# Kernel tuning notes

Measured on AMD Instinct MI355X. Metric: run time of the kernel, lower is better.

Reference implementation:

```python
import jax, jax.numpy as jnp
import numpy as np

D_MODEL, H, KV, HD = 2048, 32, 8, 64  # head_dim = 64, RoPE half-dim = 32
B, L = 2, 2048
EPS = 1e-06


def apply_rope(t, cos, sin):
    # t: [b,l,h,hd]; cos/sin: [1,l,1,hd//2] (broadcast over batch and heads)
    dim = t.shape[-1] // 2
    cos = cos[..., :dim]
    sin = sin[..., :dim]
    x1, x2 = t[..., :dim], t[..., dim:]
    return jnp.concatenate([x1 * cos - x2 * sin, x2 * cos + x1 * sin], axis=-1)


def setup_inputs() -> dict:
    key = jax.random.key(0)
    ks = jax.random.split(key, 5)
    x = jax.random.normal(ks[0], (B, L, D_MODEL), dtype=jnp.float32)
    # true rotary tables, theta=10000
    half = HD // 2
    inv_freq = 1.0 / (10000.0 ** (jnp.arange(half, dtype=jnp.float32) / half))
    ang = jnp.arange(L, dtype=jnp.float32)[:, None] * inv_freq[None, :]  # [L, half]
    cos = jnp.cos(ang)[None, :, None, :]  # [1,L,1,half]
    sin = jnp.sin(ang)[None, :, None, :]
    s = 0.02
    Wq = jax.random.normal(ks[1], (D_MODEL, D_MODEL), dtype=jnp.float32) * s
    Wk = jax.random.normal(ks[2], (D_MODEL, KV * HD), dtype=jnp.float32) * s
    Wv = jax.random.normal(ks[3], (D_MODEL, KV * HD), dtype=jnp.float32) * s
    Wo = jax.random.normal(ks[4], (D_MODEL, D_MODEL), dtype=jnp.float32) * s
    return {"x": x, "cos": cos, "sin": sin, "Wq": Wq, "Wk": Wk, "Wv": Wv, "Wo": Wo}


def reference(x, cos, sin, Wq, Wk, Wv, Wo):
    b, l, _ = x.shape
    q = (x @ Wq).reshape(b, l, H, HD)
    k = (x @ Wk).reshape(b, l, KV, HD)
    v = (x @ Wv).reshape(b, l, KV, HD)
    q = apply_rope(q, cos, sin)
    k = apply_rope(k, cos[:, :, :KV, :], sin[:, :, :KV, :])
    # QK RMS-norm (qk_norm=True path), done in fp32
    q32 = q.astype(jnp.float32)
    k32 = k.astype(jnp.float32)
    q = (q32 * jax.lax.rsqrt(jnp.mean(jnp.square(q32), axis=-1, keepdims=True) + EPS)).astype(q.dtype)
    k = (k32 * jax.lax.rsqrt(jnp.mean(jnp.square(k32), axis=-1, keepdims=True) + EPS)).astype(k.dtype)
    # GQA: repeat KV heads to match Q heads
    g = H // KV
    k = jnp.repeat(k, g, axis=2)
    v = jnp.repeat(v, g, axis=2)
    scale = jax.lax.rsqrt(jnp.float32(HD))
    scores = jnp.einsum('blhd,bmhd->bhlm', q, k) * scale  # [b,H,L,L]
    causal = jnp.tril(jnp.ones((l, l), dtype=jnp.bool_))[None, None]
    scores = jnp.where(causal, scores, jnp.full_like(scores, -10000.0))
    attn = jax.nn.softmax(scores.astype(jnp.float32), axis=-1).astype(v.dtype)
    out = jnp.einsum('bhql,blhd->bqhd', attn, v).reshape(b, l, D_MODEL)
    return out @ Wo
```

## Files before the change

### kernel.cpp

```cpp
#include <hip/hip_runtime.h>
#include <hip/hip_bf16.h>
#include <cstdint>
#include <cstddef>

#define D_MODEL 2048
#define NH 32
#define NKV 8
#define HD 64
#define BB 2
#define LL 2048
#define EPS 1e-6f
#define MM (BB * LL)
#define QS 3072
#define KO 2048
#define VO 2560

typedef __hip_bfloat16 bf16;
typedef short bf16x8 __attribute__((ext_vector_type(8)));
typedef short s16x4 __attribute__((ext_vector_type(4)));
typedef float f32x4 __attribute__((ext_vector_type(4)));

__device__ inline float4 ld_bf4u(const unsigned short* p) {
  const ushort4 u = *(const ushort4*)p;
  float4 r;
  r.x = __uint_as_float(((unsigned)u.x) << 16);
  r.y = __uint_as_float(((unsigned)u.y) << 16);
  r.z = __uint_as_float(((unsigned)u.z) << 16);
  r.w = __uint_as_float(((unsigned)u.w) << 16);
  return r;
}
__device__ inline float4 ld4_rt(const void* p, size_t i, bool f32) {
  if (f32) return *(const float4*)((const float*)p + i);
  return ld_bf4u((const unsigned short*)p + i);
}
__device__ inline float ld1_rt(const void* p, size_t i, bool f32) {
  if (f32) return ((const float*)p)[i];
  unsigned short u = ((const unsigned short*)p)[i];
  return __uint_as_float(((unsigned)u) << 16);
}
__device__ inline unsigned short f2bf(float f) {
  bf16 h = __float2bfloat16(f);
  return *reinterpret_cast<unsigned short*>(&h);
}
__device__ inline float bfu2f(unsigned short u) {
  return __uint_as_float(((unsigned)u) << 16);
}
__device__ inline void store1(float* p, float v) { *p = v; }
__device__ inline void store1(unsigned short* p, float v) { *p = f2bf(v); }

__device__ inline void glds16(const unsigned short* g, unsigned short* l) {
  __builtin_amdgcn_global_load_lds(
      (const __attribute__((address_space(1))) unsigned int*)g,
      (__attribute__((address_space(3))) unsigned int*)l, 16, 0, 0);
}

__global__ __launch_bounds__(256) void detect_all(
    const unsigned short* p0, const unsigned short* p1, const unsigned short* p2,
    const unsigned short* p3, const unsigned short* p4, const unsigned short* p5,
    const unsigned short* p6, int* __restrict__ flags) {
  const unsigned short* ptrs[7] = {p0, p1, p2, p3, p4, p5, p6};
  const int b = blockIdx.x;
  const uint4* p = (const uint4*)ptrs[b];
  __shared__ int found;
  if (threadIdx.x == 0) found = 0;
  __syncthreads();
  int loc = 0;
#pragma unroll
  for (int it = 0; it < 16; ++it) {
    uint4 v = p[it * 256 + threadIdx.x];
    unsigned wds[4] = {v.x, v.y, v.z, v.w};
#pragma unroll
    for (int q = 0; q < 4; ++q) {
      unsigned lo = wds[q] & 0xFFFFu, hi = wds[q] >> 16;
      if (((lo >> 7) & 0xFFu) == 0xFFu || ((hi >> 7) & 0xFFu) == 0xFFu) loc = 1;
    }
  }
  if (loc) atomicOr(&found, 1);
  __syncthreads();
  if (threadIdx.x == 0) flags[b] = found;
}

__global__ __launch_bounds__(256) void cvt_bf16(const void* __restrict__ src,
                                                unsigned short* __restrict__ dst,
                                                int n4, const int* __restrict__ flags, int idx) {
  const bool f32 = flags[idx] != 0;
  int i = blockIdx.x * 256 + threadIdx.x;
  if (i < n4) {
    float4 v = ld4_rt(src, (size_t)i * 4, f32);
    ushort4 o;
    o.x = f2bf(v.x); o.y = f2bf(v.y); o.z = f2bf(v.z); o.w = f2bf(v.w);
    *(ushort4*)&dst[(size_t)i * 4] = o;
  }
}

__global__ __launch_bounds__(256) void transpose_any(const void* __restrict__ src,
                                                     unsigned short* __restrict__ dst,
                                                     int K, int N,
                                                     const int* __restrict__ flags, int idx) {
  const bool f32 = flags[idx] != 0;
  __shared__ unsigned short tile[64][65];
  const int t = threadIdx.x;
  const int n0 = blockIdx.x * 64, k0 = blockIdx.y * 64;
  const int cr = t >> 4, cc = (t & 15) * 4;
#pragma unroll
  for (int rr = 0; rr < 4; ++rr) {
    int row = rr * 16 + cr;
    float4 v = ld4_rt(src, (size_t)(k0 + row) * N + n0 + cc, f32);
    tile[row][cc + 0] = f2bf(v.x);
    tile[row][cc + 1] = f2bf(v.y);
    tile[row][cc + 2] = f2bf(v.z);
    tile[row][cc + 3] = f2bf(v.w);
  }
  __syncthreads();
#pragma unroll
  for (int rr = 0; rr < 4; ++rr) {
    int nrow = rr * 16 + cr;
    ushort4 o;
    o.x = tile[cc + 0][nrow];
    o.y = tile[cc + 1][nrow];
    o.z = tile[cc + 2][nrow];
    o.w = tile[cc + 3][nrow];
    *(ushort4*)&dst[(size_t)(n0 + nrow) * K + k0 + cc] = o;
  }
}

__global__ __launch_bounds__(256) void v_to_vt(const unsigned short* __restrict__ qkv,
                                               unsigned short* __restrict__ vt) {
  __shared__ unsigned short tile[64][72];
  const int t = threadIdx.x;
  const int l0 = blockIdx.x * 64;
  const int bk = blockIdx.y;
  const int r = t >> 2, c16 = (t & 3) * 16;
  const int b = bk >> 3, kvh = bk & 7;
  const unsigned short* src = &qkv[(size_t)(b * LL + l0 + r) * QS + VO + kvh * 64 + c16];
  *(uint4*)&tile[r][c16] = *(const uint4*)&src[0];
  *(uint4*)&tile[r][c16 + 8] = *(const uint4*)&src[8];
  __syncthreads();
  unsigned short u[16];
#pragma unroll
  for (int j = 0; j < 16; ++j) u[j] = tile[c16 + j][r];
  unsigned short* dst = &vt[((size_t)bk * 64 + r) * LL + l0 + c16];
  *(uint4*)&dst[0] = *(uint4*)&u[0];
  *(uint4*)&dst[8] = *(uint4*)&u[8];
}

template <typename CT, int FUSE>
__global__ __launch_bounds__(256) void gemm_mfma(const unsigned short* __restrict__ A,
                                                 const unsigned short* __restrict__ Bt,
                                                 CT* __restrict__ C,
                                                 int M, int N, int K, int lda,
                                                 const void* __restrict__ cosp,
                                                 const void* __restrict__ sinp,
                                                 const int* __restrict__ flags) {
  __shared__ __align__(16) unsigned short As[2][128 * 32];
  __shared__ __align__(16) unsigned short Bs[2][128 * 32];
  const int t = threadIdx.x;
  const int lane = t & 63, w = t >> 6;
  const int wm = (w >> 1) * 64, wn = (w & 1) * 64;
  const int g = lane >> 4, m16 = lane & 15;
  const int nwg = gridDim.x * gridDim.y;
  const int orig = blockIdx.y * gridDim.x + blockIdx.x;
  const int swz = (orig & 7) * (nwg >> 3) + (orig >> 3);
  const int m0 = (swz / gridDim.x) * 128, n0 = (swz % gridDim.x) * 128;
  const unsigned short* gA = &A[(size_t)(m0 + (t >> 2)) * lda + (t & 3) * 8];
  const unsigned short* gB = &Bt[(size_t)(n0 + (t >> 2)) * K + (t & 3) * 8];
  const int l8 = t * 8;
  f32x4 acc[4][4] = {};
  glds16(gA, &As[0][l8]);
  glds16(gA + (size_t)64 * lda, &As[0][l8 + 2048]);
  glds16(gB, &Bs[0][l8]);
  glds16(gB + (size_t)64 * K, &Bs[0][l8 + 2048]);
  __syncthreads();
  int cur = 0;
  for (int k0 = 0; k0 < K; k0 += 32) {
    if (k0 + 32 < K) {
      glds16(gA + k0 + 32, &As[cur ^ 1][l8]);
      glds16(gA + (size_t)64 * lda + k0 + 32, &As[cur ^ 1][l8 + 2048]);
      glds16(gB + k0 + 32, &Bs[cur ^ 1][l8]);
      glds16(gB + (size_t)64 * K + k0 + 32, &Bs[cur ^ 1][l8 + 2048]);
    }
    bf16x8 af[4], bfr[4];
#pragma unroll
    for (int i = 0; i < 4; ++i) af[i] = *(const bf16x8*)&As[cur][(wm + i * 16 + m16) * 32 + g * 8];
#pragma unroll
    for (int j = 0; j < 4; ++j) bfr[j] = *(const bf16x8*)&Bs[cur][(wn + j * 16 + m16) * 32 + g * 8];
#pragma unroll
    for (int i = 0; i < 4; ++i)
#pragma unroll
      for (int j = 0; j < 4; ++j)
        acc[i][j] = __builtin_amdgcn_mfma_f32_16x16x32_bf16(af[i], bfr[j], acc[i][j], 0, 0, 0);
    __syncthreads();
    cur ^= 1;
  }
  if constexpr (FUSE) {
    const int colbase = n0 + wn;
    if (colbase < VO) {
      const bool cf = flags[1] != 0, sf = flags[2] != 0;
#pragma unroll
      for (int i = 0; i < 4; ++i)
#pragma unroll
        for (int r = 0; r < 4; ++r) {
          const int row = m0 + wm + i * 16 + g * 4 + r;
          const int l = row & (LL - 1);
          const float c0 = ld1_rt(cosp, l * 32 + m16, cf);
          const float c1 = ld1_rt(cosp, l * 32 + 16 + m16, cf);
          const float s0 = ld1_rt(sinp, l * 32 + m16, sf);
          const float s1 = ld1_rt(sinp, l * 32 + 16 + m16, sf);
          const float x0 = acc[i][0][r], x1 = acc[i][1][r];
          const float x2 = acc[i][2][r], x3 = acc[i][3][r];
          const float r0 = x0 * c0 - x2 * s0;
          const float r1 = x1 * c1 - x3 * s1;
          const float r2 = x2 * c0 + x0 * s0;
          const float r3 = x3 * c1 + x1 * s1;
          float ss = r0 * r0 + r1 * r1 + r2 * r2 + r3 * r3;
#pragma unroll
          for (int off = 1; off < 16; off <<= 1) ss += __shfl_xor(ss, off);
          const float sc = rsqrtf(ss * (1.0f / HD) + EPS);
          CT* cr = &C[(size_t)row * N + colbase + m16];
          store1(cr + 0, r0 * sc);
          store1(cr + 16, r1 * sc);
          store1(cr + 32, r2 * sc);
          store1(cr + 48, r3 * sc);
        }
      return;
    }
  }
#pragma unroll
  for (int i = 0; i < 4; ++i)
#pragma unroll
    for (int j = 0; j < 4; ++j)
#pragma unroll
      for (int r = 0; r < 4; ++r) {
        int row = m0 + wm + i * 16 + g * 4 + r;
        int col = n0 + wn + j * 16 + m16;
        store1(&C[(size_t)row * N + col], acc[i][j][r]);
      }
}

__global__ __launch_bounds__(256) void attn_mfma(unsigned short* __restrict__ qkv,
                                                 const unsigned short* __restrict__ vt) {
  __shared__ __align__(16) unsigned short Ks[2][64 * 64];
  __shared__ __align__(16) unsigned short Vs[2][64 * 64];
  __shared__ __align__(16) unsigned short Pt[4][64 * 16];
  const int t = threadIdx.x, lane = t & 63, w = t >> 6;
  const int g = lane >> 4, m16 = lane & 15;
  const int h = blockIdx.x, b = blockIdx.y;
  const int qt = (LL / 64 - 1) - blockIdx.z;
  const int kvh = h >> 2;
  const int q0 = qt * 64, qr0 = q0 + w * 16;

  bf16x8 qf0, qf1;
  {
    const unsigned short* qrow = &qkv[(size_t)(b * LL + qr0 + m16) * QS + h * 64 + g * 8];
    qf0 = *(const bf16x8*)&qrow[0];
    qf1 = *(const bf16x8*)&qrow[32];
  }
  f32x4 Oacc[4] = {};
  float lrow[4] = {0.f, 0.f, 0.f, 0.f};

  const int lr = lane >> 3;
  const int lc = (lane & 7) ^ lr;
  const unsigned short* gK = &qkv[(size_t)(b * LL) * QS + KO + kvh * 64 + lc * 8];
  const unsigned short* gV = &vt[((size_t)(b * NKV + kvh) * 64 + w * 16 + lr) * LL + lc * 8];
  const int dbase = w * 1024 + lane * 8;
  const int nIter = q0 / 64 + 1;

#pragma unroll
  for (int c = 0; c < 2; ++c) {
    glds16(gK + (size_t)(w * 16 + c * 8 + lr) * QS, &Ks[0][dbase + c * 512]);
    glds16(gV + (size_t)c * 8 * LL, &Vs[0][dbase + c * 512]);
  }
  __syncthreads();

  const int sw8 = (m16 & 7) * 8;
  for (int it = 0; it < nIter; ++it) {
    const int j0 = it * 64;
    const int cur = it & 1;
    if (it + 1 < nIter) {
      const int nj = j0 + 64;
#pragma unroll
      for (int c = 0; c < 2; ++c) {
        glds16(gK + (size_t)(nj + w * 16 + c * 8 + lr) * QS, &Ks[cur ^ 1][dbase + c * 512]);
        glds16(gV + (size_t)c * 8 * LL + nj, &Vs[cur ^ 1][dbase + c * 512]);
      }
    }
    const unsigned short* KsB = Ks[cur];
    const unsigned short* VsB = Vs[cur];

    f32x4 S[4];
#pragma unroll
    for (int jt = 0; jt < 4; ++jt) {
      const int rb = (jt * 16 + m16) * 64;
      bf16x8 kf0 = *(const bf16x8*)&KsB[rb + ((g * 8) ^ sw8)];
      bf16x8 kf1 = *(const bf16x8*)&KsB[rb + (((g + 4) * 8) ^ sw8)];
      f32x4 z = {0.f, 0.f, 0.f, 0.f};
      z = __builtin_amdgcn_mfma_f32_16x16x32_bf16(qf0, kf0, z, 0, 0, 0);
      S[jt] = __builtin_amdgcn_mfma_f32_16x16x32_bf16(qf1, kf1, z, 0, 0, 0);
    }
    if (j0 == q0) {
#pragma unroll
      for (int jt = 0; jt < 4; ++jt)
#pragma unroll
        for (int r = 0; r < 4; ++r) {
          int col = q0 + jt * 16 + m16;
          int row = qr0 + g * 4 + r;
          float p = __expf(fmaf(S[jt][r], 0.125f, -8.0f));
          p = (col <= row) ? p : 0.f;
          S[jt][r] = p;
          lrow[r] += p;
        }
    } else {
#pragma unroll
      for (int jt = 0; jt < 4; ++jt)
#pragma unroll
        for (int r = 0; r < 4; ++r) {
          float p = __expf(fmaf(S[jt][r], 0.125f, -8.0f));
          S[jt][r] = p;
          lrow[r] += p;
        }
    }
#pragma unroll
    for (int jt = 0; jt < 4; ++jt) {
      ushort4 pw;
      pw.x = f2bf(S[jt][0]); pw.y = f2bf(S[jt][1]);
      pw.z = f2bf(S[jt][2]); pw.w = f2bf(S[jt][3]);
      *(ushort4*)&Pt[w][(jt * 16 + m16) * 16 + g * 4] = pw;
    }
    s16x4 a0, a1, b0, b1;
    {
      __attribute__((address_space(3))) unsigned short* p3 =
          (__attribute__((address_space(3))) unsigned short*)&Pt[w][g * 128 + m16 * 4];
      unsigned paddr = (unsigned)(size_t)p3;
      asm volatile(
          "s_waitcnt lgkmcnt(0)\n\t"
          "ds_read_b64_tr_b16 %0, %4\n\t"
          "ds_read_b64_tr_b16 %1, %4 offset:128\n\t"
          "ds_read_b64_tr_b16 %2, %4 offset:1024\n\t"
          "ds_read_b64_tr_b16 %3, %4 offset:1152\n\t"
          "s_waitcnt lgkmcnt(0)"
          : "=&v"(a0), "=&v"(a1), "=&v"(b0), "=&v"(b1)
          : "v"(paddr)
          : "memory");
      __builtin_amdgcn_sched_barrier(0);
    }
    bf16x8 pf0 = __builtin_shufflevector(a0, a1, 0, 1, 2, 3, 4, 5, 6, 7);
    bf16x8 pf1 = __builtin_shufflevector(b0, b1, 0, 1, 2, 3, 4, 5, 6, 7);
#pragma unroll
    for (int dt = 0; dt < 4; ++dt) {
      const int rb = (dt * 16 + m16) * 64;
      bf16x8 vf0 = *(const bf16x8*)&VsB[rb + ((g * 8) ^ sw8)];
      bf16x8 vf1 = *(const bf16x8*)&VsB[rb + (((g + 4) * 8) ^ sw8)];
      Oacc[dt] = __builtin_amdgcn_mfma_f32_16x16x32_bf16(pf0, vf0, Oacc[dt], 0, 0, 0);
      Oacc[dt] = __builtin_amdgcn_mfma_f32_16x16x32_bf16(pf1, vf1, Oacc[dt], 0, 0, 0);
    }
    __syncthreads();
  }
  float inv[4];
#pragma unroll
  for (int r = 0; r < 4; ++r) {
#pragma unroll
    for (int off = 1; off < 16; off <<= 1) lrow[r] += __shfl_xor(lrow[r], off);
    inv[r] = 1.0f / lrow[r];
  }
#pragma unroll
  for (int dt = 0; dt < 4; ++dt)
#pragma unroll
    for (int r = 0; r < 4; ++r) {
      int row = qr0 + g * 4 + r;
      qkv[(size_t)(b * LL + row) * QS + h * 64 + dt * 16 + m16] = f2bf(Oacc[dt][r] * inv[r]);
    }
}

extern "C" void kernel_launch(void* const* d_in, const int* in_sizes, int n_in,
                              void* d_out, int out_size, void* d_ws, size_t ws_size,
                              hipStream_t stream) {
  const void* x = d_in[0];
  const void* cosp = d_in[1];
  const void* sinp = d_in[2];
  const void* Wq = d_in[3];
  const void* Wk = d_in[4];
  const void* Wv = d_in[5];
  const void* Wo = d_in[6];
  float* out = (float*)d_out;

  char* w0 = (char*)d_ws;
  int* flags = (int*)w0;
  unsigned short* xb = (unsigned short*)(w0 + 256);
  unsigned short* qkvb = xb + (size_t)MM * 2048;
  unsigned short* WqkvT = qkvb + (size_t)MM * QS;
  unsigned short* WoT = WqkvT + (size_t)QS * 2048;
  unsigned short* vt = WoT + (size_t)2048 * 2048;

  detect_all<<<7, 256, 0, stream>>>(
      (const unsigned short*)x, (const unsigned short*)cosp, (const unsigned short*)sinp,
      (const unsigned short*)Wq, (const unsigned short*)Wk, (const unsigned short*)Wv,
      (const unsigned short*)Wo, flags);
  cvt_bf16<<<MM * 2048 / 4 / 256, 256, 0, stream>>>(x, xb, MM * 2048 / 4, flags, 0);
  transpose_any<<<dim3(2048 / 64, 2048 / 64), 256, 0, stream>>>(Wq, WqkvT, 2048, 2048, flags, 3);
  transpose_any<<<dim3(512 / 64, 2048 / 64), 256, 0, stream>>>(Wk, WqkvT + (size_t)KO * 2048, 2048, 512, flags, 4);
  transpose_any<<<dim3(512 / 64, 2048 / 64), 256, 0, stream>>>(Wv, WqkvT + (size_t)VO * 2048, 2048, 512, flags, 5);
  transpose_any<<<dim3(2048 / 64, 2048 / 64), 256, 0, stream>>>(Wo, WoT, 2048, 2048, flags, 6);
  gemm_mfma<unsigned short, 1><<<dim3(QS / 128, MM / 128), 256, 0, stream>>>(
      xb, WqkvT, qkvb, MM, QS, 2048, 2048, cosp, sinp, flags);
  v_to_vt<<<dim3(LL / 64, BB * NKV), 256, 0, stream>>>(qkvb, vt);
  attn_mfma<<<dim3(NH, BB, LL / 64), 256, 0, stream>>>(qkvb, vt);
  gemm_mfma<float, 0><<<dim3(2048 / 128, MM / 128), 256, 0, stream>>>(
      qkvb, WoT, out, MM, 2048, 2048, QS, nullptr, nullptr, nullptr);
}
```

Measured before the change: 338.2 us.

## Triple-buffer GEMM loads, fold softmax scale into Q, batch weight transposes

New measurement: 327.5 us. 3.2% less time.

```diff
diff --git a/kernel.cpp b/kernel.cpp
--- a/kernel.cpp
+++ b/kernel.cpp
@@ -14,6 +14,8 @@
 #define QS 3072
 #define KO 2048
 #define VO 2560
+#define QSCALE 0.18033688f
+#define SM_BIAS 11.5415603f
 
 typedef __hip_bfloat16 bf16;
 typedef short bf16x8 __attribute__((ext_vector_type(8)));
@@ -93,11 +95,21 @@
   }
 }
 
-__global__ __launch_bounds__(256) void transpose_any(const void* __restrict__ src,
-                                                     unsigned short* __restrict__ dst,
-                                                     int K, int N,
-                                                     const int* __restrict__ flags, int idx) {
-  const bool f32 = flags[idx] != 0;
+__global__ __launch_bounds__(256) void transpose_all(
+    const void* __restrict__ Wq, const void* __restrict__ Wk,
+    const void* __restrict__ Wv, const void* __restrict__ Wo,
+    unsigned short* __restrict__ WqkvT, unsigned short* __restrict__ WoT,
+    const int* __restrict__ flags) {
+  const int z = blockIdx.z;
+  const void* srcs[4] = {Wq, Wk, Wv, Wo};
+  unsigned short* dsts[4] = {WqkvT, WqkvT + (size_t)KO * 2048, WqkvT + (size_t)VO * 2048, WoT};
+  const int Ns[4] = {2048, 512, 512, 2048};
+  const int N = Ns[z];
+  if (blockIdx.x * 64 >= N) return;
+  const void* src = srcs[z];
+  unsigned short* dst = dsts[z];
+  const bool f32 = flags[3 + z] != 0;
+  const int K = 2048;
   __shared__ unsigned short tile[64][65];
   const int t = threadIdx.x;
   const int n0 = blockIdx.x * 64, k0 = blockIdx.y * 64;
@@ -152,8 +164,8 @@
                                                  const void* __restrict__ cosp,
                                                  const void* __restrict__ sinp,
                                                  const int* __restrict__ flags) {
-  __shared__ __align__(16) unsigned short As[2][128 * 32];
-  __shared__ __align__(16) unsigned short Bs[2][128 * 32];
+  __shared__ __align__(16) unsigned short As[3][128 * 32];
+  __shared__ __align__(16) unsigned short Bs[3][128 * 32];
   const int t = threadIdx.x;
   const int lane = t & 63, w = t >> 6;
   const int wm = (w >> 1) * 64, wn = (w & 1) * 64;
@@ -166,36 +178,52 @@
   const unsigned short* gB = &Bt[(size_t)(n0 + (t >> 2)) * K + (t & 3) * 8];
   const int l8 = t * 8;
   f32x4 acc[4][4] = {};
-  glds16(gA, &As[0][l8]);
-  glds16(gA + (size_t)64 * lda, &As[0][l8 + 2048]);
-  glds16(gB, &Bs[0][l8]);
-  glds16(gB + (size_t)64 * K, &Bs[0][l8 + 2048]);
-  __syncthreads();
-  int cur = 0;
-  for (int k0 = 0; k0 < K; k0 += 32) {
-    if (k0 + 32 < K) {
-      glds16(gA + k0 + 32, &As[cur ^ 1][l8]);
-      glds16(gA + (size_t)64 * lda + k0 + 32, &As[cur ^ 1][l8 + 2048]);
-      glds16(gB + k0 + 32, &Bs[cur ^ 1][l8]);
-      glds16(gB + (size_t)64 * K + k0 + 32, &Bs[cur ^ 1][l8 + 2048]);
+  const int T = K >> 5;
+
+#define STAGE(k0_, buf_)                                        \
+  do {                                                          \
+    glds16(gA + (k0_), &As[buf_][l8]);                          \
+    glds16(gA + (size_t)64 * lda + (k0_), &As[buf_][l8 + 2048]);\
+    glds16(gB + (k0_), &Bs[buf_][l8]);                          \
+    glds16(gB + (size_t)64 * K + (k0_), &Bs[buf_][l8 + 2048]);  \
+  } while (0)
+
+  STAGE(0, 0);
+  STAGE(32, 1);
+  asm volatile("s_waitcnt vmcnt(4)" ::: "memory");
+  __builtin_amdgcn_s_barrier();
+
+  int buf = 0;
+  for (int tt = 0; tt < T; ++tt) {
+    const int k0 = tt << 5;
+    if (tt + 2 < T) {
+      int nb = buf + 2; if (nb >= 3) nb -= 3;
+      STAGE(k0 + 64, nb);
     }
     bf16x8 af[4], bfr[4];
 #pragma unroll
-    for (int i = 0; i < 4; ++i) af[i] = *(const bf16x8*)&As[cur][(wm + i * 16 + m16) * 32 + g * 8];
-#pragma unroll
-    for (int j = 0; j < 4; ++j) bfr[j] = *(const bf16x8*)&Bs[cur][(wn + j * 16 + m16) * 32 + g * 8];
+    for (int i = 0; i < 4; ++i) af[i] = *(const bf16x8*)&As[buf][(wm + i * 16 + m16) * 32 + g * 8];
+#pragma unroll
+    for (int j = 0; j < 4; ++j) bfr[j] = *(const bf16x8*)&Bs[buf][(wn + j * 16 + m16) * 32 + g * 8];
 #pragma unroll
     for (int i = 0; i < 4; ++i)
 #pragma unroll
       for (int j = 0; j < 4; ++j)
         acc[i][j] = __builtin_amdgcn_mfma_f32_16x16x32_bf16(af[i], bfr[j], acc[i][j], 0, 0, 0);
-    __syncthreads();
-    cur ^= 1;
-  }
+    if (tt + 1 < T) {
+      if (tt + 2 < T) asm volatile("s_waitcnt vmcnt(4)" ::: "memory");
+      else            asm volatile("s_waitcnt vmcnt(0)" ::: "memory");
+      __builtin_amdgcn_s_barrier();
+    }
+    ++buf; if (buf >= 3) buf = 0;
+  }
+#undef STAGE
+
   if constexpr (FUSE) {
     const int colbase = n0 + wn;
     if (colbase < VO) {
       const bool cf = flags[1] != 0, sf = flags[2] != 0;
+      const float post = (colbase < KO) ? QSCALE : 1.0f;
 #pragma unroll
       for (int i = 0; i < 4; ++i)
 #pragma unroll
@@ -215,7 +243,7 @@
           float ss = r0 * r0 + r1 * r1 + r2 * r2 + r3 * r3;
 #pragma unroll
           for (int off = 1; off < 16; off <<= 1) ss += __shfl_xor(ss, off);
-          const float sc = rsqrtf(ss * (1.0f / HD) + EPS);
+          const float sc = rsqrtf(ss * (1.0f / HD) + EPS) * post;
           CT* cr = &C[(size_t)row * N + colbase + m16];
           store1(cr + 0, r0 * sc);
           store1(cr + 16, r1 * sc);
@@ -304,7 +332,7 @@
         for (int r = 0; r < 4; ++r) {
           int col = q0 + jt * 16 + m16;
           int row = qr0 + g * 4 + r;
-          float p = __expf(fmaf(S[jt][r], 0.125f, -8.0f));
+          float p = exp2f(S[jt][r] - SM_BIAS);
           p = (col <= row) ? p : 0.f;
           S[jt][r] = p;
           lrow[r] += p;
@@ -314,7 +342,7 @@
       for (int jt = 0; jt < 4; ++jt)
 #pragma unroll
         for (int r = 0; r < 4; ++r) {
-          float p = __expf(fmaf(S[jt][r], 0.125f, -8.0f));
+          float p = exp2f(S[jt][r] - SM_BIAS);
           S[jt][r] = p;
           lrow[r] += p;
         }
@@ -396,10 +424,7 @@
       (const unsigned short*)Wq, (const unsigned short*)Wk, (const unsigned short*)Wv,
       (const unsigned short*)Wo, flags);
   cvt_bf16<<<MM * 2048 / 4 / 256, 256, 0, stream>>>(x, xb, MM * 2048 / 4, flags, 0);
-  transpose_any<<<dim3(2048 / 64, 2048 / 64), 256, 0, stream>>>(Wq, WqkvT, 2048, 2048, flags, 3);
-  transpose_any<<<dim3(512 / 64, 2048 / 64), 256, 0, stream>>>(Wk, WqkvT + (size_t)KO * 2048, 2048, 512, flags, 4);
-  transpose_any<<<dim3(512 / 64, 2048 / 64), 256, 0, stream>>>(Wv, WqkvT + (size_t)VO * 2048, 2048, 512, flags, 5);
-  transpose_any<<<dim3(2048 / 64, 2048 / 64), 256, 0, stream>>>(Wo, WoT, 2048, 2048, flags, 6);
+  transpose_all<<<dim3(32, 32, 4), 256, 0, stream>>>(Wq, Wk, Wv, Wo, WqkvT, WoT, flags);
   gemm_mfma<unsigned short, 1><<<dim3(QS / 128, MM / 128), 256, 0, stream>>>(
       xb, WqkvT, qkvb, MM, QS, 2048, 2048, cosp, sinp, flags);
   v_to_vt<<<dim3(LL / 64, BB * NKV), 256, 0, stream>>>(qkvb, vt);
```
